# Optimization experiments

Hardware: AMD Instinct MI355X
Metric: run time of the kernel (lower is better)

Reference implementation:

```python
import jax, jax.numpy as jnp
import numpy as np

SCALE = 10.0
DIM = 512
DIM_HEAD = 64
HEADS = DIM // DIM_HEAD
LN_EPS = 1e-05
L2_EPS = 1e-12


def l2norm(t, axis=1):
    # Faithful to source: default axis=1 (token axis for [b, n, h, d] tensors)
    denom = jnp.clip(jnp.linalg.norm(t, ord=2, axis=axis, keepdims=True), L2_EPS)
    return t / denom


def setup_inputs() -> dict:
    key = jax.random.key(0)
    k1, k2, k3 = jax.random.split(key, 3)
    B, H, W, C = 8, 32, 32, 512
    x = jax.random.normal(k1, (B, H, W, C), dtype=jnp.float32)
    ln_scale = jnp.ones((C,), dtype=jnp.float32)
    # 1x1 convs == channel matmuls; fan-in scaled init
    w_qkv = jax.random.normal(k2, (C, 3 * DIM), dtype=jnp.float32) / np.sqrt(C)
    w_out = jax.random.normal(k3, (DIM, C), dtype=jnp.float32) / np.sqrt(DIM)
    b_out = jnp.zeros((C,), dtype=jnp.float32)
    return {"x": x, "ln_scale": ln_scale, "w_qkv": w_qkv, "w_out": w_out, "b_out": b_out}


def reference(x, ln_scale, w_qkv, w_out, b_out):
    B, H, W, C = x.shape
    N = H * W
    # LayerNorm over channels (use_bias=False, use_scale=True)
    mean = jnp.mean(x, axis=-1, keepdims=True)
    var = jnp.mean(jnp.square(x - mean), axis=-1, keepdims=True)
    y = (x - mean) * jax.lax.rsqrt(var + LN_EPS) * ln_scale
    # 1x1 conv QKV projection (no bias)
    qkv = jnp.einsum('bhwc,cf->bhwf', y, w_qkv)  # [B,H,W,3*DIM]
    q, k, v = jnp.split(qkv, 3, axis=-1)
    # b x y (h d) -> b (x y) h d
    def to_tokens(t):
        return t.reshape(B, N, HEADS, DIM_HEAD)
    q, k, v = map(to_tokens, (q, k, v))
    # l2norm over axis=1 (token axis), faithful to source default
    q = l2norm(q)
    k = l2norm(k)
    sim = jnp.einsum('bihd,bjhd->bhij', q, k) * SCALE  # [B,heads,N,N]
    attn = jax.nn.softmax(sim, axis=-1)
    out = jnp.einsum('bhij,bjhd->bhid', attn, v)  # [B,heads,N,d]
    # b h (x y) d -> b x y (h d)
    out = out.transpose(0, 2, 1, 3).reshape(B, H, W, HEADS * DIM_HEAD)
    # 1x1 output conv (with bias)
    out = jnp.einsum('bhwf,fc->bhwc', out, w_out) + b_out
    return out
```

## Files before the change

kernel.cpp:

```cpp
#include <hip/hip_runtime.h>

typedef __bf16 bf16x8 __attribute__((ext_vector_type(8)));
typedef float f32x4 __attribute__((ext_vector_type(4)));

#define DEV static __device__ __forceinline__

DEV unsigned short f2bf(float f) {
    union { __bf16 h; unsigned short s; } c; c.h = (__bf16)f; return c.s;
}
DEV float bf2f(unsigned short h) {
    union { unsigned u; float f; } c; c.u = ((unsigned)h) << 16; return c.f;
}
DEV unsigned packbf2(float a, float b) {
    union { __bf16 h[2]; unsigned u; } c;
    c.h[0] = (__bf16)a; c.h[1] = (__bf16)b; return c.u;
}

DEV f32x4 mfma16(bf16x8 a, bf16x8 b, f32x4 c) {
    return __builtin_amdgcn_mfma_f32_16x16x32_bf16(a, b, c, 0, 0, 0);
}

#define GLOAD16(gp, lp)                                                        \
    __builtin_amdgcn_global_load_lds(                                          \
        (const __attribute__((address_space(1))) unsigned int*)(gp),           \
        (__attribute__((address_space(3))) unsigned int*)(lp), 16, 0, 0)

__global__ __launch_bounds__(256) void ln_conv_kernel(const float* __restrict__ x,
                                                      const float* __restrict__ lnsc,
                                                      unsigned short* __restrict__ y,
                                                      float* __restrict__ ssq,
                                                      const float* __restrict__ wqkv,
                                                      const float* __restrict__ wout,
                                                      unsigned short* __restrict__ wqkvt,
                                                      unsigned short* __restrict__ woutt) {
    const int t = threadIdx.x;
    if (blockIdx.x >= 2048) {
        const int i = (blockIdx.x - 2048) * 256 + t;
        if (i < 512 * 1536) {
            int f = i >> 9, c = i & 511;
            wqkvt[i] = f2bf(wqkv[(size_t)c * 1536 + f]);
        } else {
            int j = i - 512 * 1536;
            int n = j >> 9, k = j & 511;
            woutt[j] = f2bf(wout[(size_t)k * 512 + n]);
        }
        return;
    }
    if (blockIdx.x < 32) ssq[(blockIdx.x << 8) | t] = 0.0f;
    const int token = blockIdx.x * 4 + (t >> 6);
    const int lane = t & 63;
    const float4* xp = (const float4*)(x + (size_t)token * 512 + lane * 8);
    float4 v0 = xp[0], v1 = xp[1];
    float s = v0.x + v0.y + v0.z + v0.w + v1.x + v1.y + v1.z + v1.w;
    float s2 = v0.x * v0.x + v0.y * v0.y + v0.z * v0.z + v0.w * v0.w +
               v1.x * v1.x + v1.y * v1.y + v1.z * v1.z + v1.w * v1.w;
#pragma unroll
    for (int off = 1; off < 64; off <<= 1) {
        s += __shfl_xor(s, off);
        s2 += __shfl_xor(s2, off);
    }
    const float mean = s * (1.0f / 512.0f);
    const float var = s2 * (1.0f / 512.0f) - mean * mean;
    const float rstd = rsqrtf(var + 1e-5f);
    const float4* sp = (const float4*)(lnsc + lane * 8);
    float4 sc0 = sp[0], sc1 = sp[1];
    union { __bf16 h[8]; uint4 v; } pk;
    pk.h[0] = (__bf16)((v0.x - mean) * rstd * sc0.x);
    pk.h[1] = (__bf16)((v0.y - mean) * rstd * sc0.y);
    pk.h[2] = (__bf16)((v0.z - mean) * rstd * sc0.z);
    pk.h[3] = (__bf16)((v0.w - mean) * rstd * sc0.w);
    pk.h[4] = (__bf16)((v1.x - mean) * rstd * sc1.x);
    pk.h[5] = (__bf16)((v1.y - mean) * rstd * sc1.y);
    pk.h[6] = (__bf16)((v1.z - mean) * rstd * sc1.z);
    pk.h[7] = (__bf16)((v1.w - mean) * rstd * sc1.w);
    *(uint4*)(y + (size_t)token * 512 + lane * 8) = pk.v;
}

template <int WM, int WN, int NCOLS, bool OUT_BF16, bool BIAS, bool SSQ, bool VT>
__global__ __launch_bounds__(256) void gemm_bt(const unsigned short* __restrict__ A,
                                               const unsigned short* __restrict__ Bt,
                                               void* __restrict__ Cout,
                                               const float* __restrict__ bias,
                                               float* __restrict__ ssq,
                                               unsigned short* __restrict__ vt,
                                               int M, int K) {
    constexpr int BM = 2 * WM, BN = 2 * WN;
    constexpr int AB_BYTES = (BM + BN) * 64 * 2;
    constexpr int TT_BYTES = 128 * 136 * 2;
    constexpr int LDS_BYTES = (VT && TT_BYTES > AB_BYTES) ? TT_BYTES : AB_BYTES;
    __shared__ __align__(16) char smem[LDS_BYTES];
    unsigned short* As = (unsigned short*)smem;
    unsigned short* Bs = (unsigned short*)(smem + (size_t)BM * 64 * 2);
    const int t = threadIdx.x;
    const int w = t >> 6, lane = t & 63;
    const int g = lane >> 4, l15 = lane & 15;
    const int wr = w >> 1, wc = w & 1;
    const int bR = blockIdx.y, bC = blockIdx.x;
    f32x4 acc[WM / 16][WN / 16] = {};
    const size_t ldb = (size_t)K * 2;
    const char* Ag = (const char*)A + (size_t)bR * BM * ldb;
    const char* Bg = (const char*)Bt + (size_t)bC * BN * ldb;

    for (int kt = 0; kt < K; kt += 64) {
        __syncthreads();
#pragma unroll
        for (int i = 0; i < WM / 16; i++) {
            int o = i * 4096 + t * 16;
            int row = o >> 7, kb = (o & 127) ^ ((row & 7) << 4);
            GLOAD16(Ag + (size_t)row * ldb + (size_t)kt * 2 + kb, (char*)As + o);
        }
#pragma unroll
        for (int i = 0; i < WN / 16; i++) {
            int o = i * 4096 + t * 16;
            int row = o >> 7, kb = (o & 127) ^ ((row & 7) << 4);
            GLOAD16(Bg + (size_t)row * ldb + (size_t)kt * 2 + kb, (char*)Bs + o);
        }
        asm volatile("s_waitcnt vmcnt(0)" ::: "memory");
        __syncthreads();
#pragma unroll
        for (int kk = 0; kk < 64; kk += 32) {
            bf16x8 a[WM / 16], bb[WN / 16];
#pragma unroll
            for (int m = 0; m < WM / 16; m++) {
                int row = wr * WM + m * 16 + l15;
                int kb = ((kk + g * 8) * 2) ^ ((row & 7) << 4);
                a[m] = *(const bf16x8*)((const char*)As + row * 128 + kb);
            }
#pragma unroll
            for (int n = 0; n < WN / 16; n++) {
                int row = wc * WN + n * 16 + l15;
                int kb = ((kk + g * 8) * 2) ^ ((row & 7) << 4);
                bb[n] = *(const bf16x8*)((const char*)Bs + row * 128 + kb);
            }
#pragma unroll
            for (int m = 0; m < WM / 16; m++)
#pragma unroll
                for (int n = 0; n < WN / 16; n++)
                    acc[m][n] = mfma16(a[m], bb[n], acc[m][n]);
        }
    }
    const int rbase = bR * BM + wr * WM;
    const int cbase = bC * BN + wc * WN;
    if (!VT || bC < 8) {
#pragma unroll
        for (int m = 0; m < WM / 16; m++)
#pragma unroll
            for (int n = 0; n < WN / 16; n++)
#pragma unroll
                for (int r = 0; r < 4; r++) {
                    int row = rbase + m * 16 + g * 4 + r;
                    int col = cbase + n * 16 + l15;
                    float v = acc[m][n][r];
                    if constexpr (OUT_BF16)
                        ((unsigned short*)Cout)[(size_t)row * NCOLS + col] = f2bf(v);
                    else
                        ((float*)Cout)[(size_t)row * NCOLS + col] =
                            v + (BIAS ? bias[col] : 0.f);
                }
    }
    if constexpr (SSQ) {
        if (bC < 8) {
            const int bb2 = bR >> 3;
#pragma unroll
            for (int n = 0; n < WN / 16; n++) {
                float ps = 0.f;
#pragma unroll
                for (int m = 0; m < WM / 16; m++)
#pragma unroll
                    for (int r = 0; r < 4; r++) ps += acc[m][n][r] * acc[m][n][r];
                ps += __shfl_xor(ps, 16);
                ps += __shfl_xor(ps, 32);
                if (g == 0)
                    atomicAdd(&ssq[bb2 * 1024 + cbase + n * 16 + l15], ps);
            }
        }
    }
    if constexpr (VT) {
        if (bC >= 8) {
            unsigned short* TT = (unsigned short*)smem;
            __syncthreads();
#pragma unroll
            for (int m = 0; m < WM / 16; m++)
#pragma unroll
                for (int n = 0; n < WN / 16; n++)
#pragma unroll
                    for (int r = 0; r < 4; r++) {
                        int row = wr * WM + m * 16 + g * 4 + r;
                        int col = wc * WN + n * 16 + l15;
                        TT[col * 136 + row] = f2bf(acc[m][n][r]);
                    }
            __syncthreads();
            const int f = t >> 1, th = t & 1;
            const int fh = (bC - 8) * 128 + f;
            const int hh = fh >> 6, dd = fh & 63;
            const int bb3 = bR >> 3, nb = (bR & 7) * 128;
            unsigned short* dst =
                vt + (((size_t)bb3 * 8 + hh) * 64 + dd) * 1024 + nb + th * 64;
            const unsigned short* srcp = TT + f * 136 + th * 64;
#pragma unroll
            for (int j = 0; j < 8; j++)
                *(uint4*)(dst + j * 8) = *(const uint4*)(srcp + j * 8);
        }
    }
}

__global__ __launch_bounds__(256) void attn_kernel(const unsigned short* __restrict__ qkv,
                                                   const unsigned short* __restrict__ vt,
                                                   unsigned short* __restrict__ attnout,
                                                   const float* __restrict__ ssq) {
    __shared__ unsigned short Ks[2][4096];
    __shared__ unsigned short Vs[2][4096];
    __shared__ unsigned short Ps[4][2048];
    __shared__ float smq[64];
    const int t = threadIdx.x, w = t >> 6, lane = t & 63;
    const int g = lane >> 4, l15 = lane & 15;
    const int qt = blockIdx.x, bh = blockIdx.y;
    const int b = bh >> 3, h = bh & 7;
    const size_t qrow0 = (size_t)b * 1024 + qt * 128;
    const char* qg = (const char*)qkv;
    const char* vg = (const char*)vt;

    if (t < 64) {
        float nq = fmaxf(sqrtf(ssq[b * 1024 + h * 64 + t]), 1e-12f);
        float nk = fmaxf(sqrtf(ssq[b * 1024 + 512 + h * 64 + t]), 1e-12f);
        smq[t] = 14.42695040888963f / (nq * nk);
    }
    __syncthreads();

    bf16x8 qf[2][2];
#pragma unroll
    for (int qb = 0; qb < 2; qb++)
#pragma unroll
        for (int c = 0; c < 2; c++) {
            union { bf16x8 v; unsigned short u[8]; } in, ov;
            in.v = *(const bf16x8*)(qkv + (qrow0 + w * 32 + qb * 16 + l15) * 1536 +
                                    h * 64 + c * 32 + g * 8);
#pragma unroll
            for (int j = 0; j < 8; j++)
                ov.u[j] = f2bf(bf2f(in.u[j]) * smq[c * 32 + g * 8 + j]);
            qf[qb][c] = ov.v;
        }

    f32x4 accO[2][4] = {};
    float prs[2] = {0.f, 0.f};

#define ASTAGE(buf, tt_)                                                              \
    {                                                                                 \
        const int kt_ = (tt_) * 64;                                                   \
        _Pragma("unroll") for (int i = 0; i < 2; i++) {                               \
            int o = i * 4096 + t * 16;                                                \
            int row = o >> 7, kb = (o & 127) ^ ((row & 7) << 4);                      \
            GLOAD16(qg + ((size_t)b * 1024 + kt_ + row) * 3072 + 1024 + h * 128 + kb, \
                    (char*)Ks[buf] + o);                                              \
            GLOAD16(vg + ((size_t)bh * 64 + row) * 2048 + (size_t)kt_ * 2 + kb,       \
                    (char*)Vs[buf] + o);                                              \
        }                                                                             \
    }

    ASTAGE(0, 0)
    for (int tt = 0; tt < 16; ++tt) {
        const int cur = tt & 1;
        if (tt < 15) {
            ASTAGE(cur ^ 1, tt + 1)
            asm volatile("s_waitcnt vmcnt(4)" ::: "memory");
        } else {
            asm volatile("s_waitcnt vmcnt(0)" ::: "memory");
        }
        __builtin_amdgcn_s_barrier();

        f32x4 s[2][4] = {};
        __builtin_amdgcn_s_setprio(1);
#pragma unroll
        for (int c = 0; c < 2; c++) {
            bf16x8 bk[4];
#pragma unroll
            for (int n = 0; n < 4; n++) {
                int krow = n * 16 + l15;
                int kb = ((c * 32 + g * 8) * 2) ^ ((krow & 7) << 4);
                bk[n] = *(const bf16x8*)((const char*)Ks[cur] + krow * 128 + kb);
            }
#pragma unroll
            for (int qb = 0; qb < 2; qb++)
#pragma unroll
                for (int n = 0; n < 4; n++)
                    s[qb][n] = mfma16(bk[n], qf[qb][c], s[qb][n]);
        }
        __builtin_amdgcn_s_setprio(0);
#pragma unroll
        for (int qb = 0; qb < 2; qb++) {
            const int prow = qb * 16 + l15;
#pragma unroll
            for (int n = 0; n < 4; n++) {
                float p0 = __builtin_amdgcn_exp2f(s[qb][n][0]);
                float p1 = __builtin_amdgcn_exp2f(s[qb][n][1]);
                float p2 = __builtin_amdgcn_exp2f(s[qb][n][2]);
                float p3 = __builtin_amdgcn_exp2f(s[qb][n][3]);
                prs[qb] += (p0 + p1) + (p2 + p3);
                uint2 pk;
                pk.x = packbf2(p0, p1);
                pk.y = packbf2(p2, p3);
                int kb = ((n * 16 + g * 4) * 2) ^ ((prow & 7) << 4);
                *(uint2*)((char*)Ps[w] + prow * 128 + kb) = pk;
            }
        }
        __builtin_amdgcn_s_setprio(1);
#pragma unroll
        for (int c2 = 0; c2 < 2; c2++) {
            bf16x8 bv[4];
#pragma unroll
            for (int n = 0; n < 4; n++) {
                int vrow = n * 16 + l15;
                int kb = ((c2 * 32 + g * 8) * 2) ^ ((vrow & 7) << 4);
                bv[n] = *(const bf16x8*)((const char*)Vs[cur] + vrow * 128 + kb);
            }
#pragma unroll
            for (int qb = 0; qb < 2; qb++) {
                const int prow = qb * 16 + l15;
                int kb = ((c2 * 32 + g * 8) * 2) ^ ((prow & 7) << 4);
                bf16x8 ap = *(const bf16x8*)((const char*)Ps[w] + prow * 128 + kb);
#pragma unroll
                for (int n = 0; n < 4; n++)
                    accO[qb][n] = mfma16(ap, bv[n], accO[qb][n]);
            }
        }
        __builtin_amdgcn_s_setprio(0);
        __builtin_amdgcn_s_barrier();
    }
#undef ASTAGE
#pragma unroll
    for (int qb = 0; qb < 2; qb++) {
        float tot = prs[qb];
        tot += __shfl_xor(tot, 16);
        tot += __shfl_xor(tot, 32);
        float inv[4];
#pragma unroll
        for (int r = 0; r < 4; r++) inv[r] = 1.0f / __shfl(tot, g * 4 + r);
#pragma unroll
        for (int n = 0; n < 4; n++)
#pragma unroll
            for (int r = 0; r < 4; r++)
                attnout[(qrow0 + w * 32 + qb * 16 + g * 4 + r) * 512 + h * 64 + n * 16 +
                        l15] = f2bf(accO[qb][n][r] * inv[r]);
    }
}

extern "C" void kernel_launch(void* const* d_in, const int* in_sizes, int n_in,
                              void* d_out, int out_size, void* d_ws, size_t ws_size,
                              hipStream_t stream) {
    const float* x = (const float*)d_in[0];
    const float* ln_scale = (const float*)d_in[1];
    const float* w_qkv = (const float*)d_in[2];
    const float* w_out = (const float*)d_in[3];
    const float* b_out = (const float*)d_in[4];
    float* out = (float*)d_out;

    char* ws = (char*)d_ws;
    unsigned short* y = (unsigned short*)(ws + 0);
    unsigned short* wqkvt = (unsigned short*)(ws + 8388608);
    unsigned short* woutt = (unsigned short*)(ws + 9961472);
    unsigned short* qkv = (unsigned short*)(ws + 10485760);
    unsigned short* vt = (unsigned short*)(ws + 35651584);
    float* ssq = (float*)(ws + 44040192);
    unsigned short* attnout = (unsigned short*)(ws + 0);

    ln_conv_kernel<<<6144, 256, 0, stream>>>(x, ln_scale, y, ssq, w_qkv, w_out, wqkvt,
                                             woutt);
    gemm_bt<64, 64, 1536, true, false, true, true><<<dim3(12, 64), 256, 0, stream>>>(
        y, wqkvt, qkv, nullptr, ssq, vt, 8192, 512);
    attn_kernel<<<dim3(8, 64), 256, 0, stream>>>(qkv, vt, attnout, ssq);
    gemm_bt<32, 64, 512, false, true, false, false><<<dim3(4, 128), 256, 0, stream>>>(
        attnout, woutt, out, b_out, nullptr, nullptr, 8192, 512);
}
```

Baseline: 81.53 us.

## Double-buffer GEMM K-tiles and transpose weights through an LDS tile

The GEMM main loop now uses two LDS buffers, issuing the global-to-LDS loads for the next K-tile before computing the current one. It waits only on the older loads via a partial vmcnt, which lets memory latency overlap with MFMA work. Separately, the weight transpose/convert in the first kernel goes through a 64x65 shared tile so both reads and writes are coalesced, cutting that part of the grid from 4096 to 256 blocks. Double buffering doubles GEMM LDS use, which may reduce occupancy.

After: 78.22 us. 4.1% less time.

```diff
diff --git a/kernel.cpp b/kernel.cpp
--- a/kernel.cpp
+++ b/kernel.cpp
@@ -35,14 +35,33 @@
                                                       unsigned short* __restrict__ woutt) {
     const int t = threadIdx.x;
     if (blockIdx.x >= 2048) {
-        const int i = (blockIdx.x - 2048) * 256 + t;
-        if (i < 512 * 1536) {
-            int f = i >> 9, c = i & 511;
-            wqkvt[i] = f2bf(wqkv[(size_t)c * 1536 + f]);
+        __shared__ __bf16 tile[64][65];
+        const int wblk = blockIdx.x - 2048;
+        const float* src;
+        unsigned short* dst;
+        int ldsrc, k0, f0;
+        if (wblk < 192) {
+            src = wqkv; dst = wqkvt; ldsrc = 1536;
+            k0 = (wblk / 24) * 64; f0 = (wblk % 24) * 64;
         } else {
-            int j = i - 512 * 1536;
-            int n = j >> 9, k = j & 511;
-            woutt[j] = f2bf(wout[(size_t)k * 512 + n]);
+            int w2 = wblk - 192;
+            src = wout; dst = woutt; ldsrc = 512;
+            k0 = (w2 >> 3) * 64; f0 = (w2 & 7) * 64;
+        }
+#pragma unroll
+        for (int j = 0; j < 16; j++) {
+            int idx = t + j * 256;
+            int a = idx >> 6, b2 = idx & 63;
+            tile[b2][a] = (__bf16)src[(size_t)(k0 + a) * ldsrc + f0 + b2];
+        }
+        __syncthreads();
+#pragma unroll
+        for (int j = 0; j < 16; j++) {
+            int idx = t + j * 256;
+            int fb = idx >> 6, kc = idx & 63;
+            union { __bf16 h; unsigned short s; } cv;
+            cv.h = tile[fb][kc];
+            dst[(size_t)(f0 + fb) * 512 + k0 + kc] = cv.s;
         }
         return;
     }
@@ -85,67 +104,83 @@
                                                unsigned short* __restrict__ vt,
                                                int M, int K) {
     constexpr int BM = 2 * WM, BN = 2 * WN;
-    constexpr int AB_BYTES = (BM + BN) * 64 * 2;
-    constexpr int TT_BYTES = 128 * 136 * 2;
-    constexpr int LDS_BYTES = (VT && TT_BYTES > AB_BYTES) ? TT_BYTES : AB_BYTES;
-    __shared__ __align__(16) char smem[LDS_BYTES];
-    unsigned short* As = (unsigned short*)smem;
-    unsigned short* Bs = (unsigned short*)(smem + (size_t)BM * 64 * 2);
+    constexpr int ASZ = BM * 64 * 2, BSZ = BN * 64 * 2;
+    constexpr int NLA = WM / 16, NLB = WN / 16;
+    constexpr int DBUF = 2 * (ASZ + BSZ);
+    constexpr int TTB = VT ? 128 * 136 * 2 : 0;
+    constexpr int LDSB = DBUF > TTB ? DBUF : TTB;
+    __shared__ __align__(16) char smem[LDSB];
     const int t = threadIdx.x;
     const int w = t >> 6, lane = t & 63;
     const int g = lane >> 4, l15 = lane & 15;
     const int wr = w >> 1, wc = w & 1;
     const int bR = blockIdx.y, bC = blockIdx.x;
-    f32x4 acc[WM / 16][WN / 16] = {};
+    f32x4 acc[NLA][NLB] = {};
     const size_t ldb = (size_t)K * 2;
     const char* Ag = (const char*)A + (size_t)bR * BM * ldb;
     const char* Bg = (const char*)Bt + (size_t)bC * BN * ldb;
 
-    for (int kt = 0; kt < K; kt += 64) {
-        __syncthreads();
-#pragma unroll
-        for (int i = 0; i < WM / 16; i++) {
-            int o = i * 4096 + t * 16;
-            int row = o >> 7, kb = (o & 127) ^ ((row & 7) << 4);
-            GLOAD16(Ag + (size_t)row * ldb + (size_t)kt * 2 + kb, (char*)As + o);
-        }
-#pragma unroll
-        for (int i = 0; i < WN / 16; i++) {
-            int o = i * 4096 + t * 16;
-            int row = o >> 7, kb = (o & 127) ^ ((row & 7) << 4);
-            GLOAD16(Bg + (size_t)row * ldb + (size_t)kt * 2 + kb, (char*)Bs + o);
-        }
-        asm volatile("s_waitcnt vmcnt(0)" ::: "memory");
-        __syncthreads();
+#define GSTAGE(buf, kt_)                                                            \
+    {                                                                               \
+        char* Ad = smem + (buf) * (ASZ + BSZ);                                      \
+        char* Bd = Ad + ASZ;                                                        \
+        _Pragma("unroll") for (int i = 0; i < NLA; i++) {                           \
+            int o = i * 4096 + t * 16;                                              \
+            int row = o >> 7, kb = (o & 127) ^ ((row & 7) << 4);                    \
+            GLOAD16(Ag + (size_t)row * ldb + (size_t)(kt_) * 2 + kb, Ad + o);       \
+        }                                                                           \
+        _Pragma("unroll") for (int i = 0; i < NLB; i++) {                           \
+            int o = i * 4096 + t * 16;                                              \
+            int row = o >> 7, kb = (o & 127) ^ ((row & 7) << 4);                    \
+            GLOAD16(Bg + (size_t)row * ldb + (size_t)(kt_) * 2 + kb, Bd + o);       \
+        }                                                                           \
+    }
+
+    GSTAGE(0, 0)
+    const int NT = K >> 6;
+    for (int tt = 0; tt < NT; ++tt) {
+        const int cur = tt & 1;
+        if (tt + 1 < NT) {
+            GSTAGE(cur ^ 1, (tt + 1) * 64)
+            asm volatile("s_waitcnt vmcnt(%0)" ::"n"(NLA + NLB) : "memory");
+        } else {
+            asm volatile("s_waitcnt vmcnt(0)" ::: "memory");
+        }
+        __builtin_amdgcn_s_barrier();
+        const char* Ab = smem + cur * (ASZ + BSZ);
+        const char* Bb = Ab + ASZ;
 #pragma unroll
         for (int kk = 0; kk < 64; kk += 32) {
-            bf16x8 a[WM / 16], bb[WN / 16];
-#pragma unroll
-            for (int m = 0; m < WM / 16; m++) {
+            bf16x8 a[NLA], bb[NLB];
+#pragma unroll
+            for (int m = 0; m < NLA; m++) {
                 int row = wr * WM + m * 16 + l15;
                 int kb = ((kk + g * 8) * 2) ^ ((row & 7) << 4);
-                a[m] = *(const bf16x8*)((const char*)As + row * 128 + kb);
-            }
-#pragma unroll
-            for (int n = 0; n < WN / 16; n++) {
+                a[m] = *(const bf16x8*)(Ab + row * 128 + kb);
+            }
+#pragma unroll
+            for (int n = 0; n < NLB; n++) {
                 int row = wc * WN + n * 16 + l15;
                 int kb = ((kk + g * 8) * 2) ^ ((row & 7) << 4);
-                bb[n] = *(const bf16x8*)((const char*)Bs + row * 128 + kb);
-            }
-#pragma unroll
-            for (int m = 0; m < WM / 16; m++)
-#pragma unroll
-                for (int n = 0; n < WN / 16; n++)
+                bb[n] = *(const bf16x8*)(Bb + row * 128 + kb);
+            }
+#pragma unroll
+            for (int m = 0; m < NLA; m++)
+#pragma unroll
+                for (int n = 0; n < NLB; n++)
                     acc[m][n] = mfma16(a[m], bb[n], acc[m][n]);
         }
-    }
+        __builtin_amdgcn_s_barrier();
+    }
+#undef GSTAGE
+
     const int rbase = bR * BM + wr * WM;
     const int cbase = bC * BN + wc * WN;
     if (!VT || bC < 8) {
 #pragma unroll
-        for (int m = 0; m < WM / 16; m++)
-#pragma unroll
-            for (int n = 0; n < WN / 16; n++)
+        for (int m = 0; m < NLA; m++)
+#pragma unroll
+            for (int n = 0; n < NLB; n++)
 #pragma unroll
                 for (int r = 0; r < 4; r++) {
                     int row = rbase + m * 16 + g * 4 + r;
@@ -162,10 +197,10 @@
         if (bC < 8) {
             const int bb2 = bR >> 3;
 #pragma unroll
-            for (int n = 0; n < WN / 16; n++) {
+            for (int n = 0; n < NLB; n++) {
                 float ps = 0.f;
 #pragma unroll
-                for (int m = 0; m < WM / 16; m++)
+                for (int m = 0; m < NLA; m++)
 #pragma unroll
                     for (int r = 0; r < 4; r++) ps += acc[m][n][r] * acc[m][n][r];
                 ps += __shfl_xor(ps, 16);
@@ -180,9 +215,9 @@
             unsigned short* TT = (unsigned short*)smem;
             __syncthreads();
 #pragma unroll
-            for (int m = 0; m < WM / 16; m++)
-#pragma unroll
-                for (int n = 0; n < WN / 16; n++)
+            for (int m = 0; m < NLA; m++)
+#pragma unroll
+                for (int n = 0; n < NLB; n++)
 #pragma unroll
                     for (int r = 0; r < 4; r++) {
                         int row = wr * WM + m * 16 + g * 4 + r;
@@ -363,7 +398,7 @@
     float* ssq = (float*)(ws + 44040192);
     unsigned short* attnout = (unsigned short*)(ws + 0);
 
-    ln_conv_kernel<<<6144, 256, 0, stream>>>(x, ln_scale, y, ssq, w_qkv, w_out, wqkvt,
+    ln_conv_kernel<<<2304, 256, 0, stream>>>(x, ln_scale, y, ssq, w_qkv, w_out, wqkvt,
                                              woutt);
     gemm_bt<64, 64, 1536, true, false, true, true><<<dim3(12, 64), 256, 0, stream>>>(
         y, wqkvt, qkv, nullptr, ssq, vt, 8192, 512);
```
